# Performance work log

Hardware: AMD Instinct MI355X
Metric: run time of the kernel (lower is better)

The kernel has to match this reference:

```python
import jax, jax.numpy as jnp
import numpy as np

N_NODES = 50000
N_EDGES = 600000
IN_CH, HID_CH, OUT_CH = 128, 128, 64
N_GRAPHS = 64


def glorot(key, shape):
    fan_in, fan_out = shape
    lim = np.sqrt(6.0 / (fan_in + fan_out)).astype(np.float32)
    return jax.random.uniform(key, shape, jnp.float32, -lim, lim)


def setup_inputs() -> dict:
    key = jax.random.key(0)
    k1, k2, k3, k4, k5 = jax.random.split(key, 5)
    x = jax.random.normal(k1, (N_NODES, IN_CH), jnp.float32)
    edge_index = jax.random.randint(k2, (2, N_EDGES), 0, N_NODES, jnp.int64)
    batch = jnp.sort(jax.random.randint(k3, (N_NODES,), 0, N_GRAPHS, jnp.int64))
    W1 = glorot(k4, (IN_CH, HID_CH))
    b1 = jnp.zeros((HID_CH,), jnp.float32)
    W2 = glorot(k5, (HID_CH, OUT_CH))
    b2 = jnp.zeros((OUT_CH,), jnp.float32)
    return {"x": x, "edge_index": edge_index, "batch": batch,
            "W1": W1, "b1": b1, "W2": W2, "b2": b2}


def gcn_conv(x, edge_index, W, b):
    # PyG GCNConv: x' = D^-1/2 (A + I) D^-1/2 (x W) + b
    h = x @ W                                   # [N, F_out]
    loop = jnp.arange(N_NODES, dtype=edge_index.dtype)
    src = jnp.concatenate([edge_index[0], loop])  # [E+N]
    dst = jnp.concatenate([edge_index[1], loop])
    deg = jax.ops.segment_sum(jnp.ones_like(dst, h.dtype), dst,
                              num_segments=N_NODES)
    dinv = jnp.where(deg > 0, jax.lax.rsqrt(deg), 0.0)
    norm = dinv[src] * dinv[dst]                # [E+N]
    msg = h[src] * norm[:, None]                # gather + per-edge scale
    out = jax.ops.segment_sum(msg, dst, num_segments=N_NODES)  # scatter-add
    return out + b


def reference(x, edge_index, batch, W1, b1, W2, b2):
    h = jax.nn.relu(gcn_conv(x, edge_index, W1, b1))
    h = gcn_conv(h, edge_index, W2, b2)
    # global_add_pool: segment-sum of node features by graph id
    return jax.ops.segment_sum(h, batch, num_segments=N_GRAPHS)  # [G, OUT]
```

## Files before the change

### kernel.cpp

```cpp
#include <hip/hip_runtime.h>

#define NNODES 50000
#define NEDGES 600000
#define NGRAPHS 64
#define NBKT 196
#define EB 293
#define CHK 2048
#define GEMM_BLKS 196

typedef __attribute__((ext_vector_type(8))) short short8;
typedef __attribute__((ext_vector_type(4))) float f32x4;

__device__ inline short f2bf(float f) {
    unsigned u = __float_as_uint(f);
    u = (u + 0x7fffu + ((u >> 16) & 1u)) >> 16;
    return (short)u;
}
__device__ inline float bf2f(unsigned short s) {
    return __uint_as_float(((unsigned)s) << 16);
}
__device__ inline float bf_lo(unsigned w) { return __uint_as_float(w << 16); }
__device__ inline float bf_hi(unsigned w) { return __uint_as_float(w & 0xffff0000u); }
__device__ inline void fmabf8(const uint4 m, float n, float* a) {
    a[0] = fmaf(bf_lo(m.x), n, a[0]); a[1] = fmaf(bf_hi(m.x), n, a[1]);
    a[2] = fmaf(bf_lo(m.y), n, a[2]); a[3] = fmaf(bf_hi(m.y), n, a[3]);
    a[4] = fmaf(bf_lo(m.z), n, a[4]); a[5] = fmaf(bf_hi(m.z), n, a[5]);
    a[6] = fmaf(bf_lo(m.w), n, a[6]); a[7] = fmaf(bf_hi(m.w), n, a[7]);
}
__device__ inline void addbf8(const uint4 m, float* a) {
    a[0] += bf_lo(m.x); a[1] += bf_hi(m.x);
    a[2] += bf_lo(m.y); a[3] += bf_hi(m.y);
    a[4] += bf_lo(m.z); a[5] += bf_hi(m.z);
    a[6] += bf_lo(m.w); a[7] += bf_hi(m.w);
}

__device__ inline uint4 make_frag(const float* __restrict__ W, int M, int idx) {
    int lane = idx & 63, ks = (idx >> 6) & 3, cf = idx >> 8;
    int c = cf * 16 + (lane & 15);
    int k0 = ks * 32 + (lane >> 4) * 8;
    unsigned t[8];
    #pragma unroll
    for (int j = 0; j < 8; ++j)
        t[j] = (unsigned short)f2bf(W[(k0 + j) * M + c]);
    uint4 o;
    o.x = t[0] | (t[1] << 16);
    o.y = t[2] | (t[3] << 16);
    o.z = t[4] | (t[5] << 16);
    o.w = t[6] | (t[7] << 16);
    return o;
}

__global__ __launch_bounds__(256) void k_init0(const float* __restrict__ W1,
                                               const float* __restrict__ W2,
                                               unsigned short* __restrict__ Wf1,
                                               unsigned short* __restrict__ Wf2,
                                               float* __restrict__ dout) {
    int idx = blockIdx.x * 256 + threadIdx.x;
    if (idx < NGRAPHS * 64) dout[idx] = 0.f;
    if (idx < 2048) {
        ((uint4*)Wf1)[idx] = make_frag(W1, 128, idx);
    } else if (idx < 3072) {
        ((uint4*)Wf2)[idx - 2048] = make_frag(W2, 64, idx - 2048);
    }
}

__global__ __launch_bounds__(256) void k_mega1(const float* __restrict__ X,
                                               const unsigned short* __restrict__ Wf,
                                               unsigned short* __restrict__ Y,
                                               const int* __restrict__ ei,
                                               int* __restrict__ bh) {
    constexpr int CF = 8;
    constexpr int SLOTS = CF * 4 * 64;
    __shared__ uint4 Bl[SLOTS];
    __shared__ int hist[NBKT];
    const int tid = threadIdx.x;

    if (blockIdx.x >= GEMM_BLKS) {
        int eb = blockIdx.x - GEMM_BLKS;
        for (int i = tid; i < NBKT; i += 256) hist[i] = 0;
        __syncthreads();
        int e0 = eb * CHK;
        int e1 = min(e0 + CHK, NEDGES);
        int n4 = (e1 - e0) >> 2;
        const int4* dp = (const int4*)(ei + NEDGES + e0);
        for (int i = tid; i < n4; i += 256) {
            int4 d = dp[i];
            atomicAdd(&hist[d.x >> 8], 1);
            atomicAdd(&hist[d.y >> 8], 1);
            atomicAdd(&hist[d.z >> 8], 1);
            atomicAdd(&hist[d.w >> 8], 1);
        }
        __syncthreads();
        for (int i = tid; i < NBKT; i += 256) bh[i * EB + eb] = hist[i];
        return;
    }

    for (int i = tid; i < SLOTS; i += 256) Bl[i] = ((const uint4*)Wf)[i];
    __syncthreads();

    const short8* Bs8 = (const short8*)Bl;
    const int lane = tid & 63;
    const int wave = tid >> 6;
    const int qr = lane >> 4;
    const int cl = lane & 15;
    const int wid = blockIdx.x * 4 + wave;
    const int ngroups = (NNODES + 63) / 64;
    if (wid >= ngroups) return;

    const int base = wid * 64;
    short8 a[4][4];
    #pragma unroll
    for (int r = 0; r < 4; ++r) {
        int arow = base + r * 16 + cl;
        bool ok = arow < NNODES;
        #pragma unroll
        for (int ks = 0; ks < 4; ++ks) {
            short8 v = (short8)0;
            if (ok) {
                const float* xp = X + (long)arow * 128 + ks * 32 + qr * 8;
                float4 x0 = *reinterpret_cast<const float4*>(xp);
                float4 x1 = *reinterpret_cast<const float4*>(xp + 4);
                v[0] = f2bf(x0.x); v[1] = f2bf(x0.y); v[2] = f2bf(x0.z); v[3] = f2bf(x0.w);
                v[4] = f2bf(x1.x); v[5] = f2bf(x1.y); v[6] = f2bf(x1.z); v[7] = f2bf(x1.w);
            }
            a[r][ks] = v;
        }
    }
    f32x4 acc[4][CF];
    #pragma unroll
    for (int r = 0; r < 4; ++r)
        #pragma unroll
        for (int cf = 0; cf < CF; ++cf)
            acc[r][cf] = (f32x4){0.f, 0.f, 0.f, 0.f};
    #pragma unroll
    for (int cf = 0; cf < CF; ++cf)
        #pragma unroll
        for (int ks = 0; ks < 4; ++ks) {
            short8 b = Bs8[(cf * 4 + ks) * 64 + lane];
            #pragma unroll
            for (int r = 0; r < 4; ++r)
                acc[r][cf] = __builtin_amdgcn_mfma_f32_16x16x32_bf16(a[r][ks], b, acc[r][cf], 0, 0, 0);
        }
    #pragma unroll
    for (int r = 0; r < 4; ++r) {
        int row0 = base + r * 16 + qr * 4;
        #pragma unroll
        for (int i = 0; i < 4; ++i) {
            int row = row0 + i;
            if (row < NNODES) {
                #pragma unroll
                for (int cf = 0; cf < CF; ++cf)
                    Y[(long)row * 128 + cf * 16 + cl] = (unsigned short)f2bf(acc[r][cf][i]);
            }
        }
    }
}

__global__ __launch_bounds__(512) void k_scanA1(int* __restrict__ bh,
                                                int* __restrict__ bt) {
    __shared__ int s[512];
    int b = blockIdx.x;
    int t = threadIdx.x;
    int v = (t < EB) ? bh[b * EB + t] : 0;
    s[t] = v;
    __syncthreads();
    for (int off = 1; off < 512; off <<= 1) {
        int u = (t >= off) ? s[t - off] : 0;
        __syncthreads();
        s[t] += u;
        __syncthreads();
    }
    if (t < EB) bh[b * EB + t] = s[t] - v;
    if (t == EB - 1) bt[b] = s[t];
}

__global__ __launch_bounds__(256) void k_passA2(const int* __restrict__ ei,
                                                const int* __restrict__ bh,
                                                const int* __restrict__ bt,
                                                int2* __restrict__ parted) {
    __shared__ int sc[256];
    __shared__ int cur[NBKT];
    int eb = blockIdx.x;
    int t = threadIdx.x;
    int v = (t < NBKT) ? bt[t] : 0;
    sc[t] = v;
    __syncthreads();
    for (int off = 1; off < 256; off <<= 1) {
        int u = (t >= off) ? sc[t - off] : 0;
        __syncthreads();
        sc[t] += u;
        __syncthreads();
    }
    if (t < NBKT) cur[t] = (sc[t] - v) + bh[t * EB + eb];
    __syncthreads();
    int e0 = eb * CHK;
    int e1 = min(e0 + CHK, NEDGES);
    int n4 = (e1 - e0) >> 2;
    const int4* sp = (const int4*)(ei + e0);
    const int4* dp = (const int4*)(ei + NEDGES + e0);
    for (int i = t; i < n4; i += 256) {
        int4 sv = sp[i];
        int4 dv = dp[i];
        int p0 = atomicAdd(&cur[dv.x >> 8], 1); parted[p0] = make_int2(sv.x, dv.x);
        int p1 = atomicAdd(&cur[dv.y >> 8], 1); parted[p1] = make_int2(sv.y, dv.y);
        int p2 = atomicAdd(&cur[dv.z >> 8], 1); parted[p2] = make_int2(sv.z, dv.z);
        int p3 = atomicAdd(&cur[dv.w >> 8], 1); parted[p3] = make_int2(sv.w, dv.w);
    }
}

__global__ __launch_bounds__(256) void k_passB(const int* __restrict__ bt,
                                               const int2* __restrict__ parted,
                                               int* __restrict__ rp,
                                               int* __restrict__ csr,
                                               float* __restrict__ dinv) {
    __shared__ int cnt2[256], cur[256], sc[256];
    int b = blockIdx.x;
    int t = threadIdx.x;
    int v = (t < NBKT) ? bt[t] : 0;
    sc[t] = v;
    __syncthreads();
    for (int o = 1; o < 256; o <<= 1) {
        int u = (t >= o) ? sc[t - o] : 0;
        __syncthreads();
        sc[t] += u;
        __syncthreads();
    }
    __shared__ int lo_sh, hi_sh;
    if (t == b) { lo_sh = sc[t] - v; hi_sh = sc[t]; }
    __syncthreads();
    int lo = lo_sh, hi = hi_sh;
    cnt2[t] = 0;
    __syncthreads();
    for (int i = lo + t; i < hi; i += 256)
        atomicAdd(&cnt2[parted[i].y & 255], 1);
    __syncthreads();
    sc[t] = cnt2[t];
    __syncthreads();
    for (int o = 1; o < 256; o <<= 1) {
        int u = (t >= o) ? sc[t - o] : 0;
        __syncthreads();
        sc[t] += u;
        __syncthreads();
    }
    int excl = sc[t] - cnt2[t];
    cur[t] = excl;
    int vtx = b * 256 + t;
    if (vtx < NNODES) {
        rp[vtx] = lo + excl;
        dinv[vtx] = rsqrtf((float)cnt2[t] + 1.0f);
    } else if (vtx == NNODES) {
        rp[vtx] = lo + excl;
    }
    __syncthreads();
    for (int i = lo + t; i < hi; i += 256) {
        int2 e = parted[i];
        int pos = lo + atomicAdd(&cur[e.y & 255], 1);
        csr[pos] = e.x;
    }
}

__global__ __launch_bounds__(256) void k_gather_gemm(const int* __restrict__ rp,
                                                     const int* __restrict__ csr_src,
                                                     const float* __restrict__ dinv,
                                                     const unsigned short* __restrict__ Hs,
                                                     const float* __restrict__ b1,
                                                     const unsigned short* __restrict__ Wf2,
                                                     unsigned short* __restrict__ Y) {
    __shared__ unsigned short h1[64 * 128];
    const int tid = threadIdx.x;
    const int lane = tid & 63;
    const int wave = tid >> 6;

    const int grp = lane >> 4;
    const int ln = lane & 15;
    const int c8 = ln * 8;
    const int base = blockIdx.x * 64;
    const uint4* Hp = (const uint4*)Hs;
    float4 bv0 = *reinterpret_cast<const float4*>(b1 + c8);
    float4 bv1 = *reinterpret_cast<const float4*>(b1 + c8 + 4);
    float bb[8] = {bv0.x, bv0.y, bv0.z, bv0.w, bv1.x, bv1.y, bv1.z, bv1.w};

    #pragma unroll
    for (int p = 0; p < 4; ++p) {
        int vloc = wave * 16 + p * 4 + grp;
        int v = base + vloc;
        uint4 o = {0u, 0u, 0u, 0u};
        if (v < NNODES) {
            float a[8] = {0, 0, 0, 0, 0, 0, 0, 0};
            float dd = dinv[v];
            fmabf8(Hp[((long)v * 128 + c8) >> 3], dd, a);
            int lo = rp[v], hi = rp[v + 1];
            int i = lo;
            for (; i + 4 <= hi; i += 4) {
                int s0 = csr_src[i], s1 = csr_src[i + 1];
                int s2 = csr_src[i + 2], s3 = csr_src[i + 3];
                float n0 = dinv[s0], n1 = dinv[s1], n2 = dinv[s2], n3 = dinv[s3];
                uint4 m0 = Hp[((long)s0 * 128 + c8) >> 3];
                uint4 m1 = Hp[((long)s1 * 128 + c8) >> 3];
                uint4 m2 = Hp[((long)s2 * 128 + c8) >> 3];
                uint4 m3 = Hp[((long)s3 * 128 + c8) >> 3];
                fmabf8(m0, n0, a); fmabf8(m1, n1, a);
                fmabf8(m2, n2, a); fmabf8(m3, n3, a);
            }
            for (; i < hi; ++i) {
                int s = csr_src[i];
                fmabf8(Hp[((long)s * 128 + c8) >> 3], dinv[s], a);
            }
            unsigned t[8];
            #pragma unroll
            for (int j = 0; j < 8; ++j) {
                float y = fmaxf(fmaf(a[j], dd, bb[j]), 0.f);
                t[j] = (unsigned short)f2bf(y);
            }
            o.x = t[0] | (t[1] << 16);
            o.y = t[2] | (t[3] << 16);
            o.z = t[4] | (t[5] << 16);
            o.w = t[6] | (t[7] << 16);
        }
        int byte = (vloc * 256 + c8 * 2) ^ ((vloc & 7) << 4);
        *reinterpret_cast<uint4*>((char*)h1 + byte) = o;
    }
    __syncthreads();

    const int qr = lane >> 4;
    const int cl = lane & 15;
    const int arow = wave * 16 + cl;
    short8 afr[4];
    #pragma unroll
    for (int ks = 0; ks < 4; ++ks) {
        int byte = (arow * 256 + (ks * 32 + qr * 8) * 2) ^ ((arow & 7) << 4);
        afr[ks] = *reinterpret_cast<const short8*>((const char*)h1 + byte);
    }
    const short8* Bs8 = (const short8*)Wf2;
    f32x4 acc[4];
    #pragma unroll
    for (int cf = 0; cf < 4; ++cf) acc[cf] = (f32x4){0.f, 0.f, 0.f, 0.f};
    #pragma unroll
    for (int cf = 0; cf < 4; ++cf)
        #pragma unroll
        for (int ks = 0; ks < 4; ++ks)
            acc[cf] = __builtin_amdgcn_mfma_f32_16x16x32_bf16(afr[ks], Bs8[(cf * 4 + ks) * 64 + lane], acc[cf], 0, 0, 0);
    #pragma unroll
    for (int i = 0; i < 4; ++i) {
        int row = base + wave * 16 + qr * 4 + i;
        if (row < NNODES) {
            float dv = dinv[row];
            #pragma unroll
            for (int cf = 0; cf < 4; ++cf)
                Y[(long)row * 64 + cf * 16 + cl] = (unsigned short)f2bf(acc[cf][i] * dv);
        }
    }
}

__global__ __launch_bounds__(256) void k_gather2(const int* __restrict__ rp,
                                                 const int* __restrict__ csr_src,
                                                 const float* __restrict__ dinv,
                                                 const unsigned short* __restrict__ Hs,
                                                 const float* __restrict__ bias,
                                                 unsigned short* __restrict__ out) {
    int lane = threadIdx.x & 7;
    int grp = threadIdx.x >> 3;
    int v = blockIdx.x * 32 + grp;
    if (v >= NNODES) return;
    int c8 = lane * 8;
    float dd = dinv[v];
    float a[8] = {0, 0, 0, 0, 0, 0, 0, 0};
    const uint4* Hp = (const uint4*)Hs;
    addbf8(Hp[((long)v * 64 + c8) >> 3], a);
    int lo = rp[v], hi = rp[v + 1];
    int i = lo;
    for (; i + 4 <= hi; i += 4) {
        int s0 = csr_src[i], s1 = csr_src[i + 1], s2 = csr_src[i + 2], s3 = csr_src[i + 3];
        uint4 m0 = Hp[((long)s0 * 64 + c8) >> 3];
        uint4 m1 = Hp[((long)s1 * 64 + c8) >> 3];
        uint4 m2 = Hp[((long)s2 * 64 + c8) >> 3];
        uint4 m3 = Hp[((long)s3 * 64 + c8) >> 3];
        addbf8(m0, a); addbf8(m1, a); addbf8(m2, a); addbf8(m3, a);
    }
    for (; i < hi; ++i)
        addbf8(Hp[((long)csr_src[i] * 64 + c8) >> 3], a);
    unsigned t[8];
    #pragma unroll
    for (int j = 0; j < 8; ++j)
        t[j] = (unsigned short)f2bf(fmaf(a[j], dd, bias[c8 + j]));
    uint4 o;
    o.x = t[0] | (t[1] << 16);
    o.y = t[2] | (t[3] << 16);
    o.z = t[4] | (t[5] << 16);
    o.w = t[6] | (t[7] << 16);
    ((uint4*)out)[((long)v * 64 + c8) >> 3] = o;
}

__device__ inline int lower_bound_i(const int* a, int n, int key) {
    int lo = 0, hi = n;
    while (lo < hi) {
        int mid = (lo + hi) >> 1;
        if (a[mid] < key) lo = mid + 1; else hi = mid;
    }
    return lo;
}

__global__ __launch_bounds__(256) void k_pool(const unsigned short* __restrict__ h2,
                                              const int* __restrict__ batch,
                                              float* __restrict__ out) {
    int g = blockIdx.x >> 4;
    int slice = blockIdx.x & 15;
    int lo = lower_bound_i(batch, NNODES, g);
    int hi = lower_bound_i(batch, NNODES, g + 1);
    int ch = threadIdx.x & 63;
    int part = threadIdx.x >> 6;
    float acc = 0.f;
    for (int v = lo + slice * 4 + part; v < hi; v += 64)
        acc += bf2f(h2[(long)v * 64 + ch]);
    __shared__ float red[256];
    red[threadIdx.x] = acc;
    __syncthreads();
    if (part == 0) {
        float s = red[ch] + red[64 + ch] + red[128 + ch] + red[192 + ch];
        atomicAdd(&out[g * 64 + ch], s);
    }
}

extern "C" void kernel_launch(void* const* d_in, const int* in_sizes, int n_in,
                              void* d_out, int out_size, void* d_ws, size_t ws_size,
                              hipStream_t stream) {
    const float* x   = (const float*)d_in[0];
    const int* ei    = (const int*)d_in[1];
    const int* batch = (const int*)d_in[2];
    const float* W1  = (const float*)d_in[3];
    const float* b1  = (const float*)d_in[4];
    const float* W2  = (const float*)d_in[5];
    const float* b2  = (const float*)d_in[6];
    float* out = (float*)d_out;

    char* ws = (char*)d_ws;
    float* dinv = (float*)ws;
    int*   rp   = (int*)(ws + (256 << 10));
    int*   bh   = (int*)(ws + (512 << 10));
    int*   bt   = (int*)(ws + (768 << 10));
    int*   csr  = (int*)(ws + (1u << 20));
    unsigned short* Wf1 = (unsigned short*)(ws + (3584u << 10));
    unsigned short* Wf2 = (unsigned short*)(ws + (3584u << 10) + (32 << 10));
    unsigned short* bufA = (unsigned short*)(ws + (4u << 20));
    unsigned short* bufB = (unsigned short*)(ws + (4u << 20) + (size_t)NNODES * 128 * 2);
    int2* parted = (int2*)bufB;

    k_init0<<<16, 256, 0, stream>>>(W1, W2, Wf1, Wf2, out);

    k_mega1<<<GEMM_BLKS + EB, 256, 0, stream>>>(x, Wf1, bufA, ei, bh);

    k_scanA1<<<NBKT, 512, 0, stream>>>(bh, bt);

    k_passA2<<<EB, 256, 0, stream>>>(ei, bh, bt, parted);
    k_passB<<<NBKT, 256, 0, stream>>>(bt, parted, rp, csr, dinv);

    k_gather_gemm<<<(NNODES + 63) / 64, 256, 0, stream>>>(rp, csr, dinv, bufA, b1, Wf2, bufB);

    k_gather2<<<(NNODES + 31) / 32, 256, 0, stream>>>(rp, csr, dinv, bufB, b2, bufA);

    k_pool<<<NGRAPHS * 16, 256, 0, stream>>>(bufA, batch, out);
}
```

Measured before the change: 98.18 us.

## Fuse second-layer gather with global add pooling via shared-memory graph accumulators

Merges the layer-2 neighbor aggregation kernel and the pooling kernel into one. Each block handles 256 nodes, keeps per-thread partial sums while consecutive nodes share a graph id, and flushes them into a shared-memory [64x64] accumulator. Only nonzero slots within the block's graph range are then atomically added to the output. This removes the bf16 intermediate write and re-read of h2, one kernel launch, and the pool's binary searches. In exchange the grid drops to about 196 blocks with 8 nodes per thread group, which lowers parallelism for the latency-bound gather.

```diff
diff --git a/kernel.cpp b/kernel.cpp
--- a/kernel.cpp
+++ b/kernel.cpp
@@ -15,9 +15,6 @@
     unsigned u = __float_as_uint(f);
     u = (u + 0x7fffu + ((u >> 16) & 1u)) >> 16;
     return (short)u;
-}
-__device__ inline float bf2f(unsigned short s) {
-    return __uint_as_float(((unsigned)s) << 16);
 }
 __device__ inline float bf_lo(unsigned w) { return __uint_as_float(w << 16); }
 __device__ inline float bf_hi(unsigned w) { return __uint_as_float(w & 0xffff0000u); }
@@ -306,16 +303,16 @@
                 int s = csr_src[i];
                 fmabf8(Hp[((long)s * 128 + c8) >> 3], dinv[s], a);
             }
-            unsigned t[8];
+            unsigned t8[8];
             #pragma unroll
             for (int j = 0; j < 8; ++j) {
                 float y = fmaxf(fmaf(a[j], dd, bb[j]), 0.f);
-                t[j] = (unsigned short)f2bf(y);
-            }
-            o.x = t[0] | (t[1] << 16);
-            o.y = t[2] | (t[3] << 16);
-            o.z = t[4] | (t[5] << 16);
-            o.w = t[6] | (t[7] << 16);
+                t8[j] = (unsigned short)f2bf(y);
+            }
+            o.x = t8[0] | (t8[1] << 16);
+            o.y = t8[2] | (t8[3] << 16);
+            o.z = t8[4] | (t8[5] << 16);
+            o.w = t8[6] | (t8[7] << 16);
         }
         int byte = (vloc * 256 + c8 * 2) ^ ((vloc & 7) << 4);
         *reinterpret_cast<uint4*>((char*)h1 + byte) = o;
@@ -352,72 +349,76 @@
     }
 }
 
-__global__ __launch_bounds__(256) void k_gather2(const int* __restrict__ rp,
-                                                 const int* __restrict__ csr_src,
-                                                 const float* __restrict__ dinv,
-                                                 const unsigned short* __restrict__ Hs,
-                                                 const float* __restrict__ bias,
-                                                 unsigned short* __restrict__ out) {
-    int lane = threadIdx.x & 7;
-    int grp = threadIdx.x >> 3;
-    int v = blockIdx.x * 32 + grp;
-    if (v >= NNODES) return;
-    int c8 = lane * 8;
-    float dd = dinv[v];
-    float a[8] = {0, 0, 0, 0, 0, 0, 0, 0};
+__global__ __launch_bounds__(256) void k_gather2_pool(const int* __restrict__ rp,
+                                                      const int* __restrict__ csr_src,
+                                                      const float* __restrict__ dinv,
+                                                      const unsigned short* __restrict__ Hs,
+                                                      const float* __restrict__ bias,
+                                                      const int* __restrict__ batch,
+                                                      float* __restrict__ out) {
+    __shared__ float acc_sh[NGRAPHS * 64];
+    const int tid = threadIdx.x;
+    for (int i = tid; i < NGRAPHS * 64; i += 256) acc_sh[i] = 0.f;
+    __syncthreads();
+
+    const int lane = tid & 7;
+    const int grp = tid >> 3;
+    const int c8 = lane * 8;
+    const int base = blockIdx.x * 256;
     const uint4* Hp = (const uint4*)Hs;
-    addbf8(Hp[((long)v * 64 + c8) >> 3], a);
-    int lo = rp[v], hi = rp[v + 1];
-    int i = lo;
-    for (; i + 4 <= hi; i += 4) {
-        int s0 = csr_src[i], s1 = csr_src[i + 1], s2 = csr_src[i + 2], s3 = csr_src[i + 3];
-        uint4 m0 = Hp[((long)s0 * 64 + c8) >> 3];
-        uint4 m1 = Hp[((long)s1 * 64 + c8) >> 3];
-        uint4 m2 = Hp[((long)s2 * 64 + c8) >> 3];
-        uint4 m3 = Hp[((long)s3 * 64 + c8) >> 3];
-        addbf8(m0, a); addbf8(m1, a); addbf8(m2, a); addbf8(m3, a);
-    }
-    for (; i < hi; ++i)
-        addbf8(Hp[((long)csr_src[i] * 64 + c8) >> 3], a);
-    unsigned t[8];
-    #pragma unroll
-    for (int j = 0; j < 8; ++j)
-        t[j] = (unsigned short)f2bf(fmaf(a[j], dd, bias[c8 + j]));
-    uint4 o;
-    o.x = t[0] | (t[1] << 16);
-    o.y = t[2] | (t[3] << 16);
-    o.z = t[4] | (t[5] << 16);
-    o.w = t[6] | (t[7] << 16);
-    ((uint4*)out)[((long)v * 64 + c8) >> 3] = o;
-}
-
-__device__ inline int lower_bound_i(const int* a, int n, int key) {
-    int lo = 0, hi = n;
-    while (lo < hi) {
-        int mid = (lo + hi) >> 1;
-        if (a[mid] < key) lo = mid + 1; else hi = mid;
-    }
-    return lo;
-}
-
-__global__ __launch_bounds__(256) void k_pool(const unsigned short* __restrict__ h2,
-                                              const int* __restrict__ batch,
-                                              float* __restrict__ out) {
-    int g = blockIdx.x >> 4;
-    int slice = blockIdx.x & 15;
-    int lo = lower_bound_i(batch, NNODES, g);
-    int hi = lower_bound_i(batch, NNODES, g + 1);
-    int ch = threadIdx.x & 63;
-    int part = threadIdx.x >> 6;
-    float acc = 0.f;
-    for (int v = lo + slice * 4 + part; v < hi; v += 64)
-        acc += bf2f(h2[(long)v * 64 + ch]);
-    __shared__ float red[256];
-    red[threadIdx.x] = acc;
-    __syncthreads();
-    if (part == 0) {
-        float s = red[ch] + red[64 + ch] + red[128 + ch] + red[192 + ch];
-        atomicAdd(&out[g * 64 + ch], s);
+    float4 bv0 = *reinterpret_cast<const float4*>(bias + c8);
+    float4 bv1 = *reinterpret_cast<const float4*>(bias + c8 + 4);
+    float bb[8] = {bv0.x, bv0.y, bv0.z, bv0.w, bv1.x, bv1.y, bv1.z, bv1.w};
+
+    float loc[8] = {0, 0, 0, 0, 0, 0, 0, 0};
+    int curg = -1;
+    for (int p = 0; p < 8; ++p) {
+        int v = base + p * 32 + grp;
+        if (v >= NNODES) break;
+        int g = batch[v];
+        if (g != curg) {
+            if (curg >= 0) {
+                #pragma unroll
+                for (int j = 0; j < 8; ++j)
+                    atomicAdd(&acc_sh[curg * 64 + c8 + j], loc[j]);
+            }
+            curg = g;
+            #pragma unroll
+            for (int j = 0; j < 8; ++j) loc[j] = 0.f;
+        }
+        float dd = dinv[v];
+        float a[8] = {0, 0, 0, 0, 0, 0, 0, 0};
+        addbf8(Hp[((long)v * 64 + c8) >> 3], a);
+        int lo = rp[v], hi = rp[v + 1];
+        int i = lo;
+        for (; i + 4 <= hi; i += 4) {
+            int s0 = csr_src[i], s1 = csr_src[i + 1];
+            int s2 = csr_src[i + 2], s3 = csr_src[i + 3];
+            uint4 m0 = Hp[((long)s0 * 64 + c8) >> 3];
+            uint4 m1 = Hp[((long)s1 * 64 + c8) >> 3];
+            uint4 m2 = Hp[((long)s2 * 64 + c8) >> 3];
+            uint4 m3 = Hp[((long)s3 * 64 + c8) >> 3];
+            addbf8(m0, a); addbf8(m1, a); addbf8(m2, a); addbf8(m3, a);
+        }
+        for (; i < hi; ++i)
+            addbf8(Hp[((long)csr_src[i] * 64 + c8) >> 3], a);
+        #pragma unroll
+        for (int j = 0; j < 8; ++j)
+            loc[j] += fmaf(a[j], dd, bb[j]);
+    }
+    if (curg >= 0) {
+        #pragma unroll
+        for (int j = 0; j < 8; ++j)
+            atomicAdd(&acc_sh[curg * 64 + c8 + j], loc[j]);
+    }
+    __syncthreads();
+
+    int g0 = batch[min(base, NNODES - 1)];
+    int g1 = batch[min(base + 255, NNODES - 1)];
+    int slots = (g1 - g0 + 1) * 64;
+    for (int i = tid; i < slots; i += 256) {
+        float v = acc_sh[g0 * 64 + i];
+        if (v != 0.f) atomicAdd(&out[g0 * 64 + i], v);
     }
 }
 
@@ -456,7 +457,5 @@
 
     k_gather_gemm<<<(NNODES + 63) / 64, 256, 0, stream>>>(rp, csr, dinv, bufA, b1, Wf2, bufB);
 
-    k_gather2<<<(NNODES + 31) / 32, 256, 0, stream>>>(rp, csr, dinv, bufB, b2, bufA);
-
-    k_pool<<<NGRAPHS * 16, 256, 0, stream>>>(bufA, batch, out);
-}
+    k_gather2_pool<<<(NNODES + 255) / 256, 256, 0, stream>>>(rp, csr, dinv, bufB, b2, batch, out);
+}
```

After: 120.5 us. +22.7%, slower.
